# Performance work log

Measured on AMD Instinct MI355X. Metric: run time of the kernel, lower is better.

## Reference

```python
import jax, jax.numpy as jnp
import numpy as np

D_MODEL = 1024

def setup_inputs() -> dict:
    key = jax.random.key(0)
    ks = jax.random.split(key, 7)
    B, S, D = 4, 2048, D_MODEL
    scale = 1.0 / np.sqrt(D)
    x = jax.random.normal(ks[0], (B, S, D), dtype=jnp.float32)
    Wq = jax.random.normal(ks[1], (D, D), dtype=jnp.float32) * scale
    bq = jax.random.normal(ks[2], (D,), dtype=jnp.float32) * 0.02
    Wk = jax.random.normal(ks[3], (D, D), dtype=jnp.float32) * scale
    bk = jax.random.normal(ks[4], (D,), dtype=jnp.float32) * 0.02
    Wv = jax.random.normal(ks[5], (D, D), dtype=jnp.float32) * scale
    bv = jax.random.normal(ks[6], (D,), dtype=jnp.float32) * 0.02
    return {"x": x, "Wq": Wq, "bq": bq, "Wk": Wk, "bk": bk, "Wv": Wv, "bv": bv}

def reference(x, Wq, bq, Wk, bk, Wv, bv):
    # x: [B, S, D]
    B, S, D = x.shape
    q = jnp.einsum('bsd,de->bse', x, Wq) + bq
    k = jnp.einsum('bsd,de,->bse'.replace(',->', '->'), x, Wk) + bk
    v = jnp.einsum('bsd,de->bse', x, Wv) + bv
    # scores: [B, S, S], scaled by 1/sqrt(d_model) with additive causal mask
    scores = jnp.einsum('bqd,bkd->bqk', q, k) / jnp.sqrt(jnp.float32(D))
    causal = jnp.triu(jnp.full((S, S), -jnp.inf, dtype=scores.dtype), k=1)
    probs = jax.nn.softmax(scores + causal, axis=-1)
    return jnp.einsum('bqk,bkd->bqd', probs, v)
```

## Files before the change

kernel.cpp:

```cpp
#include <hip/hip_runtime.h>
#include <hip/hip_bf16.h>

#define S_LEN 2048
#define DM 1024
#define NB 4

typedef __attribute__((ext_vector_type(8))) short short8;
typedef __attribute__((ext_vector_type(4))) short short4v;
typedef __attribute__((ext_vector_type(4))) float floatx4;

__device__ inline short f2bf(float f) {
    union { float f; unsigned u; } v; v.f = f;
    unsigned r = 0x7fffu + ((v.u >> 16) & 1u);
    return (short)((v.u + r) >> 16);
}

__device__ inline void load16(const short* g, short* l) {
    __builtin_amdgcn_global_load_lds(
        (const __attribute__((address_space(1))) void*)g,
        (__attribute__((address_space(3))) void*)l,
        16, 0, 0);
}

__device__ inline void gemm_core(const short* __restrict__ A,
                                 const short* __restrict__ Bt,
                                 int lda, int ldb, int kLen,
                                 int m0, int n0, floatx4 acc[4][4],
                                 short* As, short* Bs) {
    const int tid  = threadIdx.x;
    const int lane = tid & 63;
    const int wave = tid >> 6;
    const int wr   = (wave >> 1) * 64;
    const int wc   = (wave & 1) * 64;
    const int quad = lane >> 4;
    const int l16  = lane & 15;

    const int r0  = wave * 32 + (lane >> 2);
    const int r1  = r0 + 16;
    const int kc  = (lane & 3) ^ ((r0 >> 1) & 3);
    const short* gA0 = A  + (size_t)(m0 + r0) * lda + kc * 8;
    const short* gA1 = A  + (size_t)(m0 + r1) * lda + kc * 8;
    const short* gB0 = Bt + (size_t)(n0 + r0) * ldb + kc * 8;
    const short* gB1 = Bt + (size_t)(n0 + r1) * ldb + kc * 8;
    short* lA0 = &As[(wave * 2 + 0) * 512];
    short* lA1 = &As[(wave * 2 + 1) * 512];
    short* lB0 = &Bs[(wave * 2 + 0) * 512];
    short* lB1 = &Bs[(wave * 2 + 1) * 512];

    const short* fa[4];
    const short* fb[4];
#pragma unroll
    for (int t = 0; t < 4; t++) {
        int ra = wr + t * 16 + l16;
        fa[t] = &As[ra * 32 + (quad ^ ((ra >> 1) & 3)) * 8];
        int rb = wc + t * 16 + l16;
        fb[t] = &Bs[rb * 32 + (quad ^ ((rb >> 1) & 3)) * 8];
    }

    for (int k0 = 0; k0 < kLen; k0 += 32) {
        load16(gA0, lA0);
        load16(gA1, lA1);
        load16(gB0, lB0);
        load16(gB1, lB1);
        gA0 += 32; gA1 += 32; gB0 += 32; gB1 += 32;
        __syncthreads();

        short8 af[4], bf[4];
#pragma unroll
        for (int t = 0; t < 4; t++) af[t] = *(const short8*)fa[t];
#pragma unroll
        for (int t = 0; t < 4; t++) bf[t] = *(const short8*)fb[t];
#pragma unroll
        for (int mt = 0; mt < 4; mt++)
#pragma unroll
            for (int nt = 0; nt < 4; nt++)
                acc[mt][nt] = __builtin_amdgcn_mfma_f32_16x16x32_bf16(
                    af[mt], bf[nt], acc[mt][nt], 0, 0, 0);
        __syncthreads();
    }
}

__global__ void prep(const float* __restrict__ x,
                     const float* __restrict__ Wq, const float* __restrict__ Wk,
                     const float* __restrict__ Wv,
                     short* __restrict__ xb, short* __restrict__ Wt,
                     float* __restrict__ denom) {
    __shared__ float t[64][65];
    int bid = blockIdx.x, tid = threadIdx.x;
    if (bid < 768) {
        int w = bid >> 8, tl = bid & 255;
        const float* W = (w == 0) ? Wq : (w == 1) ? Wk : Wv;
        short* out = Wt + (size_t)w * DM * DM;
        int bx = (tl & 15) * 64;
        int by = (tl >> 4) * 64;
        int tx = tid & 63, ty = tid >> 6;
        for (int r = ty; r < 64; r += 4)
            t[r][tx] = W[(size_t)(by + r) * DM + bx + tx];
        __syncthreads();
        for (int r = ty; r < 64; r += 4)
            out[(size_t)(bx + r) * DM + by + tx] = f2bf(t[tx][r]);
    } else if (bid < 768 + 8192) {
        int i = (bid - 768) * 256 + tid;
        float4 v = ((const float4*)x)[i];
        short4v o;
        o.x = f2bf(v.x); o.y = f2bf(v.y); o.z = f2bf(v.z); o.w = f2bf(v.w);
        ((short4v*)xb)[i] = o;
    } else {
        int i = (bid - 8960) * 256 + tid;
        if (i < NB * S_LEN) denom[i] = 0.f;
    }
}

__global__ __launch_bounds__(256, 4)
void qkv_gemm(const short* __restrict__ xb, const short* __restrict__ Wt,
              const float* __restrict__ bq, const float* __restrict__ bk,
              const float* __restrict__ bv,
              short* __restrict__ Qb, short* __restrict__ Kb,
              short* __restrict__ Vtb) {
    __shared__ short As[4608];
    __shared__ short Bs[4608];
    int w = 2 - (int)blockIdx.z;
    int n0 = blockIdx.x * 128;
    int m0 = blockIdx.y * 128;
    const short* Bt = Wt + (size_t)w * DM * DM;
    const float* bias = (w == 0) ? bq : (w == 1) ? bk : bv;

    floatx4 acc[4][4];
#pragma unroll
    for (int i = 0; i < 4; i++)
#pragma unroll
        for (int j = 0; j < 4; j++) acc[i][j] = (floatx4){0.f, 0.f, 0.f, 0.f};

    gemm_core(xb, Bt, DM, DM, DM, m0, n0, acc, As, Bs);

    const int lane = threadIdx.x & 63, wave = threadIdx.x >> 6;
    const int wr = (wave >> 1) * 64, wc = (wave & 1) * 64;
    const int quad = lane >> 4, l16 = lane & 15;

    if (w < 2) {
        short* out = w ? Kb : Qb;
        float scale = w ? 1.0f : 0.03125f;
#pragma unroll
        for (int mt = 0; mt < 4; mt++)
#pragma unroll
            for (int nt = 0; nt < 4; nt++) {
                int col = n0 + wc + nt * 16 + l16;
                float bv_ = bias[col];
#pragma unroll
                for (int r = 0; r < 4; r++) {
                    int row = m0 + wr + mt * 16 + quad * 4 + r;
                    out[(size_t)row * DM + col] = f2bf((acc[mt][nt][r] + bv_) * scale);
                }
            }
    } else {
        int b = m0 >> 11;
        int sbase = (m0 & 2047) + wr;
        float bvv[4];
#pragma unroll
        for (int nt = 0; nt < 4; nt++) bvv[nt] = bias[n0 + wc + nt * 16 + l16];
        short* buf = (wave & 1) ? Bs : As;
        short* vt = Vtb + ((size_t)b * DM + n0 + wc) * S_LEN;
#pragma unroll
        for (int p = 0; p < 2; p++) {
            __syncthreads();
            if ((wave >> 1) == p) {
#pragma unroll
                for (int mt = 0; mt < 4; mt++)
#pragma unroll
                    for (int nt = 0; nt < 4; nt++) {
                        int c = nt * 16 + l16;
                        short4v pk;
                        pk.x = f2bf(acc[mt][nt][0] + bvv[nt]);
                        pk.y = f2bf(acc[mt][nt][1] + bvv[nt]);
                        pk.z = f2bf(acc[mt][nt][2] + bvv[nt]);
                        pk.w = f2bf(acc[mt][nt][3] + bvv[nt]);
                        *(short4v*)&buf[c * 72 + mt * 16 + quad * 4] = pk;
                    }
                asm volatile("s_waitcnt lgkmcnt(0)" ::: "memory");
#pragma unroll
                for (int ps = 0; ps < 8; ps++) {
                    int dl = ps * 8 + (lane >> 3);
                    int sl = (lane & 7) * 8;
                    short8 row = *(short8*)&buf[dl * 72 + sl];
                    *(short8*)(vt + (size_t)dl * S_LEN + sbase + sl) = row;
                }
            }
        }
    }
}

__global__ __launch_bounds__(256, 4)
void score_gemm(const short* __restrict__ Qb, const short* __restrict__ Kb,
                short* __restrict__ P, float* __restrict__ denom) {
    __shared__ short As[4096];
    __shared__ short Bs[4096];
    int b = blockIdx.z;
    int xq = blockIdx.x;
    int it = (int)((sqrtf(8.0f * xq + 1.0f) - 1.0f) * 0.5f);
    while ((it + 1) * (it + 2) / 2 <= xq) it++;
    while (it * (it + 1) / 2 > xq) it--;
    int jt = xq - it * (it + 1) / 2;
    int n0 = jt * 128, m0 = it * 128;
    const short* A  = Qb + (size_t)b * S_LEN * DM;
    const short* Bt = Kb + (size_t)b * S_LEN * DM;

    floatx4 acc[4][4];
#pragma unroll
    for (int i = 0; i < 4; i++)
#pragma unroll
        for (int j = 0; j < 4; j++) acc[i][j] = (floatx4){0.f, 0.f, 0.f, 0.f};

    gemm_core(A, Bt, DM, DM, DM, m0, n0, acc, As, Bs);

    short* out = P + (size_t)b * S_LEN * S_LEN;
    float* dsum = denom + (size_t)b * S_LEN;
    const int lane = threadIdx.x & 63, wave = threadIdx.x >> 6;
    const int wr = (wave >> 1) * 64, wc = (wave & 1) * 64;
    const int quad = lane >> 4, l16 = lane & 15;
    const bool diag = (jt == it);
#pragma unroll
    for (int mt = 0; mt < 4; mt++) {
#pragma unroll
        for (int r = 0; r < 4; r++) {
            int row = m0 + wr + mt * 16 + quad * 4 + r;
            float psum = 0.f;
#pragma unroll
            for (int nt = 0; nt < 4; nt++) {
                int col = n0 + wc + nt * 16 + l16;
                float e = __expf(acc[mt][nt][r]);
                if (diag && col > row) e = 0.f;
                out[(size_t)row * S_LEN + col] = f2bf(e);
                psum += e;
            }
#pragma unroll
            for (int off = 8; off > 0; off >>= 1)
                psum += __shfl_down(psum, off, 16);
            if (l16 == 0) atomicAdd(&dsum[row], psum);
        }
    }
}

__global__ __launch_bounds__(256, 4)
void pv_gemm(const short* __restrict__ P, const short* __restrict__ Vtb,
             const float* __restrict__ denom, float* __restrict__ O) {
    __shared__ short As[4096];
    __shared__ short Bs[4096];
    int b = blockIdx.z;
    int n0 = blockIdx.x * 128;
    int it = (int)(gridDim.y - 1 - blockIdx.y);
    int m0 = it * 128;
    int kLen = (it + 1) * 128;
    const short* A  = P   + (size_t)b * S_LEN * S_LEN;
    const short* Bt = Vtb + (size_t)b * DM * S_LEN;

    floatx4 acc[4][4];
#pragma unroll
    for (int i = 0; i < 4; i++)
#pragma unroll
        for (int j = 0; j < 4; j++) acc[i][j] = (floatx4){0.f, 0.f, 0.f, 0.f};

    gemm_core(A, Bt, S_LEN, S_LEN, kLen, m0, n0, acc, As, Bs);

    float* out = O + (size_t)b * S_LEN * DM;
    const float* dsum = denom + (size_t)b * S_LEN;
    const int lane = threadIdx.x & 63, wave = threadIdx.x >> 6;
    const int wr = (wave >> 1) * 64, wc = (wave & 1) * 64;
    const int quad = lane >> 4, l16 = lane & 15;
#pragma unroll
    for (int mt = 0; mt < 4; mt++) {
#pragma unroll
        for (int r = 0; r < 4; r++) {
            int row = m0 + wr + mt * 16 + quad * 4 + r;
            float inv = 1.0f / dsum[row];
#pragma unroll
            for (int nt = 0; nt < 4; nt++) {
                int col = n0 + wc + nt * 16 + l16;
                out[(size_t)row * DM + col] = acc[mt][nt][r] * inv;
            }
        }
    }
}

extern "C" void kernel_launch(void* const* d_in, const int* in_sizes, int n_in,
                              void* d_out, int out_size, void* d_ws, size_t ws_size,
                              hipStream_t stream) {
    const float* x  = (const float*)d_in[0];
    const float* Wq = (const float*)d_in[1];
    const float* bq = (const float*)d_in[2];
    const float* Wk = (const float*)d_in[3];
    const float* bk = (const float*)d_in[4];
    const float* Wv = (const float*)d_in[5];
    const float* bv = (const float*)d_in[6];
    float* out = (float*)d_out;

    char* ws = (char*)d_ws;
    const size_t MB = 1u << 20;
    short* xb    = (short*)(ws + 0);
    short* Wt    = (short*)(ws + 16 * MB);
    short* Qb    = (short*)(ws + 22 * MB);
    short* Kb    = (short*)(ws + 38 * MB);
    short* Vtb   = (short*)(ws + 54 * MB);
    short* P     = (short*)(ws + 70 * MB);
    float* denom = (float*)(ws + 102 * MB);

    prep<<<dim3(8992), dim3(256), 0, stream>>>(x, Wq, Wk, Wv, xb, Wt, denom);
    qkv_gemm<<<dim3(8, 64, 3), dim3(256), 0, stream>>>(xb, Wt, bq, bk, bv, Qb, Kb, Vtb);
    score_gemm<<<dim3(136, 1, NB), dim3(256), 0, stream>>>(Qb, Kb, P, denom);
    pv_gemm<<<dim3(8, 16, NB), dim3(256), 0, stream>>>(P, Vtb, denom, out);
}
```

Measured before the change: 254.7 us.

## Fuse Q, K, V projections into one kernel sharing the x tile

Replaces the three-way grid over Q/K/V weight matrices with a single kernel where each block loads the x tile once and computes all three projections against it, with an inlined K-loop. This removes redundant loads of x and cuts the block count to a third. In exchange it triples the accumulator registers (48 float4 per thread) and the shared memory for B, and lowers launch bounds to 2 blocks per CU, which reduces occupancy and the grid to 512 blocks.

Result: faster. 235.8 us (-7.4%).

```diff
diff --git a/kernel.cpp b/kernel.cpp
--- a/kernel.cpp
+++ b/kernel.cpp
@@ -111,34 +111,88 @@
     }
 }
 
-__global__ __launch_bounds__(256, 4)
-void qkv_gemm(const short* __restrict__ xb, const short* __restrict__ Wt,
-              const float* __restrict__ bq, const float* __restrict__ bk,
-              const float* __restrict__ bv,
-              short* __restrict__ Qb, short* __restrict__ Kb,
-              short* __restrict__ Vtb) {
+__global__ __launch_bounds__(256, 2)
+void qkv_fused(const short* __restrict__ xb, const short* __restrict__ Wt,
+               const float* __restrict__ bq, const float* __restrict__ bk,
+               const float* __restrict__ bv,
+               short* __restrict__ Qb, short* __restrict__ Kb,
+               short* __restrict__ Vtb) {
     __shared__ short As[4608];
-    __shared__ short Bs[4608];
-    int w = 2 - (int)blockIdx.z;
+    __shared__ short Bs[3 * 4608];
     int n0 = blockIdx.x * 128;
     int m0 = blockIdx.y * 128;
-    const short* Bt = Wt + (size_t)w * DM * DM;
-    const float* bias = (w == 0) ? bq : (w == 1) ? bk : bv;
-
-    floatx4 acc[4][4];
-#pragma unroll
-    for (int i = 0; i < 4; i++)
-#pragma unroll
-        for (int j = 0; j < 4; j++) acc[i][j] = (floatx4){0.f, 0.f, 0.f, 0.f};
-
-    gemm_core(xb, Bt, DM, DM, DM, m0, n0, acc, As, Bs);
-
-    const int lane = threadIdx.x & 63, wave = threadIdx.x >> 6;
-    const int wr = (wave >> 1) * 64, wc = (wave & 1) * 64;
-    const int quad = lane >> 4, l16 = lane & 15;
-
-    if (w < 2) {
+
+    const int tid  = threadIdx.x;
+    const int lane = tid & 63;
+    const int wave = tid >> 6;
+    const int wr   = (wave >> 1) * 64;
+    const int wc   = (wave & 1) * 64;
+    const int quad = lane >> 4;
+    const int l16  = lane & 15;
+
+    floatx4 acc[3][4][4];
+#pragma unroll
+    for (int w = 0; w < 3; w++)
+#pragma unroll
+        for (int i = 0; i < 4; i++)
+#pragma unroll
+            for (int j = 0; j < 4; j++) acc[w][i][j] = (floatx4){0.f, 0.f, 0.f, 0.f};
+
+    const int r0 = wave * 32 + (lane >> 2);
+    const int r1 = r0 + 16;
+    const int kc = (lane & 3) ^ ((r0 >> 1) & 3);
+    const short* gA0 = xb + (size_t)(m0 + r0) * DM + kc * 8;
+    const short* gA1 = xb + (size_t)(m0 + r1) * DM + kc * 8;
+    const short* gW0 = Wt + (size_t)(n0 + r0) * DM + kc * 8;
+    const short* gW1 = Wt + (size_t)(n0 + r1) * DM + kc * 8;
+    short* lA0 = &As[(wave * 2 + 0) * 512];
+    short* lA1 = &As[(wave * 2 + 1) * 512];
+    short* lB0 = &Bs[(wave * 2 + 0) * 512];
+    short* lB1 = &Bs[(wave * 2 + 1) * 512];
+
+    const short* fa[4];
+    const short* fb[4];
+#pragma unroll
+    for (int t = 0; t < 4; t++) {
+        int ra = wr + t * 16 + l16;
+        fa[t] = &As[ra * 32 + (quad ^ ((ra >> 1) & 3)) * 8];
+        int rb = wc + t * 16 + l16;
+        fb[t] = &Bs[rb * 32 + (quad ^ ((rb >> 1) & 3)) * 8];
+    }
+
+    for (int k0 = 0; k0 < DM; k0 += 32) {
+        load16(gA0, lA0);
+        load16(gA1, lA1);
+#pragma unroll
+        for (int w = 0; w < 3; w++) {
+            load16(gW0 + (size_t)w * DM * DM, lB0 + w * 4608);
+            load16(gW1 + (size_t)w * DM * DM, lB1 + w * 4608);
+        }
+        gA0 += 32; gA1 += 32; gW0 += 32; gW1 += 32;
+        __syncthreads();
+
+        short8 af[4];
+#pragma unroll
+        for (int t = 0; t < 4; t++) af[t] = *(const short8*)fa[t];
+#pragma unroll
+        for (int w = 0; w < 3; w++) {
+            short8 bf[4];
+#pragma unroll
+            for (int t = 0; t < 4; t++) bf[t] = *(const short8*)(fb[t] + w * 4608);
+#pragma unroll
+            for (int mt = 0; mt < 4; mt++)
+#pragma unroll
+                for (int nt = 0; nt < 4; nt++)
+                    acc[w][mt][nt] = __builtin_amdgcn_mfma_f32_16x16x32_bf16(
+                        af[mt], bf[nt], acc[w][mt][nt], 0, 0, 0);
+        }
+        __syncthreads();
+    }
+
+#pragma unroll
+    for (int w = 0; w < 2; w++) {
         short* out = w ? Kb : Qb;
+        const float* bias = w ? bk : bq;
         float scale = w ? 1.0f : 0.03125f;
 #pragma unroll
         for (int mt = 0; mt < 4; mt++)
@@ -149,15 +203,17 @@
 #pragma unroll
                 for (int r = 0; r < 4; r++) {
                     int row = m0 + wr + mt * 16 + quad * 4 + r;
-                    out[(size_t)row * DM + col] = f2bf((acc[mt][nt][r] + bv_) * scale);
+                    out[(size_t)row * DM + col] = f2bf((acc[w][mt][nt][r] + bv_) * scale);
                 }
             }
-    } else {
+    }
+
+    {
         int b = m0 >> 11;
         int sbase = (m0 & 2047) + wr;
         float bvv[4];
 #pragma unroll
-        for (int nt = 0; nt < 4; nt++) bvv[nt] = bias[n0 + wc + nt * 16 + l16];
+        for (int nt = 0; nt < 4; nt++) bvv[nt] = bv[n0 + wc + nt * 16 + l16];
         short* buf = (wave & 1) ? Bs : As;
         short* vt = Vtb + ((size_t)b * DM + n0 + wc) * S_LEN;
 #pragma unroll
@@ -170,10 +226,10 @@
                     for (int nt = 0; nt < 4; nt++) {
                         int c = nt * 16 + l16;
                         short4v pk;
-                        pk.x = f2bf(acc[mt][nt][0] + bvv[nt]);
-                        pk.y = f2bf(acc[mt][nt][1] + bvv[nt]);
-                        pk.z = f2bf(acc[mt][nt][2] + bvv[nt]);
-                        pk.w = f2bf(acc[mt][nt][3] + bvv[nt]);
+                        pk.x = f2bf(acc[2][mt][nt][0] + bvv[nt]);
+                        pk.y = f2bf(acc[2][mt][nt][1] + bvv[nt]);
+                        pk.z = f2bf(acc[2][mt][nt][2] + bvv[nt]);
+                        pk.w = f2bf(acc[2][mt][nt][3] + bvv[nt]);
                         *(short4v*)&buf[c * 72 + mt * 16 + quad * 4] = pk;
                     }
                 asm volatile("s_waitcnt lgkmcnt(0)" ::: "memory");
@@ -304,7 +360,7 @@
     float* denom = (float*)(ws + 102 * MB);
 
     prep<<<dim3(8992), dim3(256), 0, stream>>>(x, Wq, Wk, Wv, xb, Wt, denom);
-    qkv_gemm<<<dim3(8, 64, 3), dim3(256), 0, stream>>>(xb, Wt, bq, bk, bv, Qb, Kb, Vtb);
+    qkv_fused<<<dim3(8, 64), dim3(256), 0, stream>>>(xb, Wt, bq, bk, bv, Qb, Kb, Vtb);
     score_gemm<<<dim3(136, 1, NB), dim3(256), 0, stream>>>(Qb, Kb, P, denom);
     pv_gemm<<<dim3(8, 16, NB), dim3(256), 0, stream>>>(P, Vtb, denom, out);
 }
```
